# Optimization experiments

Measured on AMD Instinct MI355X. Metric: run time of the kernel, lower is better.

## Reference

```python
import jax, jax.numpy as jnp
import numpy as np

N_USERS = 100000
N_ITEMS = 50000
N_NODES = N_USERS + N_ITEMS
EMB_DIM = 64
NNZ = 4800000
BATCH = 4096
N_LAYERS = 3


def setup_inputs() -> dict:
    key = jax.random.key(0)
    k1, k2, k3, k4, k5, k6, k7, k8 = jax.random.split(key, 8)
    edge_row = jax.random.randint(k1, (NNZ,), 0, N_NODES, dtype=jnp.int32)
    edge_col = jax.random.randint(k2, (NNZ,), 0, N_NODES, dtype=jnp.int32)
    # normalized adjacency values are positive, ~1/sqrt(deg_i*deg_j)
    edge_val = jax.random.uniform(k3, (NNZ,), dtype=jnp.float32) * (2.0 / 32.0)
    user_emb = jax.random.normal(k4, (N_USERS, EMB_DIM), dtype=jnp.float32) * 0.1
    item_emb = jax.random.normal(k5, (N_ITEMS, EMB_DIM), dtype=jnp.float32) * 0.1
    users = jax.random.randint(k6, (BATCH,), 0, N_USERS, dtype=jnp.int64)
    pos_items = jax.random.randint(k7, (BATCH,), 0, N_ITEMS, dtype=jnp.int64)
    neg_items = jax.random.randint(k8, (BATCH,), 0, N_ITEMS, dtype=jnp.int64)
    return {
        "edge_row": edge_row,
        "edge_col": edge_col,
        "edge_val": edge_val,
        "user_emb": user_emb,
        "item_emb": item_emb,
        "users": users,
        "pos_items": pos_items,
        "neg_items": neg_items,
    }


def reference(edge_row, edge_col, edge_val, user_emb, item_emb, users, pos_items, neg_items):
    n_users = user_emb.shape[0]
    n_nodes = n_users + item_emb.shape[0]
    # ego embeddings: [N, D]
    ego = jnp.concatenate([user_emb, item_emb], axis=0)
    acc = ego  # running sum over layers (layer 0 included)
    for _ in range(N_LAYERS):
        # SpMM: out[r] = sum_{e: row[e]==r} val[e] * ego[col[e]]
        msg = edge_val[:, None] * ego[edge_col]          # [nnz, D]
        ego = jax.ops.segment_sum(msg, edge_row, num_segments=n_nodes)
        acc = acc + ego
    all_emb = acc / (N_LAYERS + 1)                       # layer average
    u_all = all_emb[:n_users]
    i_all = all_emb[n_users:]
    u_g = u_all[users]
    pos_i_g = i_all[pos_items]
    neg_i_g = i_all[neg_items]
    return (u_g, pos_i_g, neg_i_g)
```

## Files before the change

kernel.cpp:

```cpp
#include <hip/hip_runtime.h>

#define N_USERS 100000
#define N_ITEMS 50000
#define N_NODES 150000
#define EMB 64
#define NNZ_TOT 4800000
#define BATCH_SZ 4096

#define BROWS 64
#define NB 2344
#define CHUNKS 512
#define CHUNKE 9375
#define SBUF 3072
#define KBINS 2048
#define BIN_LDS (2 * NB * 4 + CHUNKE * 8)
#define QSCALE 262144.0f
#define QINV   3.814697265625e-6f

typedef unsigned short u16;

static __device__ __forceinline__ u16 f2bf(float f) {
    unsigned u = __float_as_uint(f);
    unsigned r = u + 0x7FFFu + ((u >> 16) & 1u);
    return (u16)(r >> 16);
}
static __device__ __forceinline__ float bf2f(u16 h) {
    return __uint_as_float(((unsigned)h) << 16);
}

__global__ void k_init(const float* __restrict__ ue, const float* __restrict__ ie,
                       u16* __restrict__ ego) {
    size_t i = (size_t)blockIdx.x * blockDim.x + threadIdx.x;
    const size_t n4 = (size_t)N_NODES * EMB / 4;
    if (i >= n4) return;
    const size_t u4 = (size_t)N_USERS * EMB / 4;
    float4 v = (i < u4) ? ((const float4*)ue)[i] : ((const float4*)ie)[i - u4];
    ushort4 o;
    o.x = f2bf(v.x); o.y = f2bf(v.y); o.z = f2bf(v.z); o.w = f2bf(v.w);
    ((ushort4*)ego)[i] = o;
}

__global__ void k_zero(int* __restrict__ p, int n) {
    int i = blockIdx.x * blockDim.x + threadIdx.x;
    if (i < n) p[i] = 0;
}

__global__ __launch_bounds__(1024) void k_bin(const int* __restrict__ erow,
                                              const int* __restrict__ ecol,
                                              const float* __restrict__ eval_,
                                              int2* __restrict__ pairsA,
                                              int* __restrict__ off_t,
                                              int* __restrict__ bucketCnt) {
    extern __shared__ int smem[];
    int*  hist = smem;
    int*  fill = smem + NB;
    int2* buf  = (int2*)(smem + 2 * NB);
    const int c = blockIdx.x;
    const int cbase = c * CHUNKE;
    const int tid = threadIdx.x;

    for (int i = tid; i < NB; i += 1024) hist[i] = 0;
    __syncthreads();

    for (int i = tid; i < CHUNKE; i += 1024)
        atomicAdd(&hist[erow[cbase + i] >> 6], 1);
    __syncthreads();

    if (tid < 64) {
        int carry = 0;
        for (int blk = 0; blk < (NB + 63) / 64; ++blk) {
            int idx = blk * 64 + tid;
            int v = (idx < NB) ? hist[idx] : 0;
            int s = v;
            #pragma unroll
            for (int o = 1; o < 64; o <<= 1) {
                int t = __shfl_up(s, o);
                if (tid >= o) s += t;
            }
            if (idx < NB) fill[idx] = s - v + carry;
            carry += __shfl(s, 63);
        }
    }
    __syncthreads();

    for (int i = tid; i < NB; i += 1024) {
        off_t[i * CHUNKS + c] = cbase + fill[i];
        atomicAdd(&bucketCnt[i], hist[i]);
    }
    if (tid == 0) off_t[NB * CHUNKS + c] = cbase + CHUNKE;
    __syncthreads();

    for (int i = tid; i < CHUNKE; i += 1024) {
        int e = cbase + i;
        int r = erow[e];
        int bb = r >> 6;
        int p = atomicAdd(&fill[bb], 1);
        int2 pr;
        pr.x = ((r & 63) << 18) | ecol[e];
        pr.y = __float_as_int(eval_[e]);
        buf[p] = pr;
    }
    __syncthreads();

    for (int i = tid; i < CHUNKE; i += 1024)
        pairsA[cbase + i] = buf[i];
}

__global__ __launch_bounds__(1024) void k_bscan(const int* __restrict__ cnt,
                                                int* __restrict__ bbase,
                                                int* __restrict__ rowptr) {
    __shared__ int lds[1024];
    const int tid = threadIdx.x;
    int vals[3];
    int local = 0;
    #pragma unroll
    for (int j = 0; j < 3; ++j) {
        int idx = tid * 3 + j;
        int v = (idx < NB) ? cnt[idx] : 0;
        vals[j] = local;
        local += v;
    }
    lds[tid] = local;
    __syncthreads();
    for (int off = 1; off < 1024; off <<= 1) {
        int t = (tid >= off) ? lds[tid - off] : 0;
        __syncthreads();
        lds[tid] += t;
        __syncthreads();
    }
    int excl = lds[tid] - local;
    #pragma unroll
    for (int j = 0; j < 3; ++j) {
        int idx = tid * 3 + j;
        if (idx <= NB) {
            int b = excl + vals[j];
            bbase[idx] = b;
            if (idx == NB) rowptr[N_NODES] = b;
        }
    }
}

__global__ __launch_bounds__(256) void k_sort(const int* __restrict__ off_t,
                                              const int2* __restrict__ pairsA,
                                              const int* __restrict__ bbase,
                                              unsigned* __restrict__ pairsB,
                                              int* __restrict__ rowptr) {
    __shared__ int hist[KBINS];
    __shared__ int fillx[KBINS];
    __shared__ int2 buf[SBUF];
    __shared__ int wsum[4];
    const int b = blockIdx.x;
    const int tid = threadIdx.x, lane = tid & 63, w = tid >> 6;

    const int s0 = off_t[b * CHUNKS + tid];
    const int e0 = off_t[(b + 1) * CHUNKS + tid];
    const int s1 = off_t[b * CHUNKS + tid + 256];
    const int e1 = off_t[(b + 1) * CHUNKS + tid + 256];
    const int l0 = e0 - s0;
    const int len = l0 + (e1 - s1);

    for (int i = tid; i < KBINS; i += 256) hist[i] = 0;

    int sc = len;
    #pragma unroll
    for (int o = 1; o < 64; o <<= 1) {
        int t = __shfl_up(sc, o);
        if (lane >= o) sc += t;
    }
    if (lane == 63) wsum[w] = sc;
    __syncthreads();
    int wbase = 0;
    for (int i = 0; i < w; ++i) wbase += wsum[i];
    int tbase = wbase + sc - len;

    for (int i = 0; i < len; ++i) {
        int2 p = (i < l0) ? pairsA[s0 + i] : pairsA[s1 + (i - l0)];
        int dst = tbase + i;
        if (dst < SBUF) buf[dst] = p;
        atomicAdd(&hist[(p.x >> 13) & (KBINS - 1)], 1);
    }
    __syncthreads();

    const int base = bbase[b];
    if (tid < 64) {
        int carry = 0;
        for (int blk = 0; blk < KBINS / 64; ++blk) {
            int idx = blk * 64 + tid;
            int v = hist[idx];
            int s2 = v;
            #pragma unroll
            for (int o = 1; o < 64; o <<= 1) {
                int t = __shfl_up(s2, o);
                if (tid >= o) s2 += t;
            }
            int excl = s2 - v + carry;
            fillx[idx] = excl;
            if ((idx & 31) == 0) {
                int node = b * BROWS + (idx >> 5);
                if (node < N_NODES) rowptr[node] = base + excl;
            }
            carry += __shfl(s2, 63);
        }
    }
    __syncthreads();

    int total = bbase[b + 1] - base;
    if (total > SBUF) total = SBUF;
    for (int i = tid; i < total; i += 256) {
        int2 p = buf[i];
        int pos = atomicAdd(&fillx[(p.x >> 13) & (KBINS - 1)], 1);
        float v = __uint_as_float((unsigned)p.y);
        unsigned q = (unsigned)(v * QSCALE);
        if (q > 16383u) q = 16383u;
        pairsB[base + pos] = (q << 18) | ((unsigned)p.x & 0x3FFFFu);
    }
}

__global__ __launch_bounds__(256) void k_spmv(const int* __restrict__ rowptr,
                                              const unsigned* __restrict__ pairs,
                                              const u16* __restrict__ cur,
                                              u16* __restrict__ nxt) {
    size_t gid = (size_t)blockIdx.x * blockDim.x + threadIdx.x;
    int pr   = (int)(gid >> 6);
    int lane = (int)(gid & 63);
    int rowA = pr * 2;
    if (rowA >= N_NODES) return;
    const int      sl  = lane & 31;
    const bool     hi  = lane >= 32;
    const unsigned sl4 = (unsigned)sl << 2;
    const char* tab = (const char*)cur;
    const uint2* p2 = (const uint2*)pairs;

    int sA = rowptr[rowA];
    int mA = rowptr[rowA + 1];
    int eBnd = rowptr[rowA + 2];

    float a0 = 0.f, a1 = 0.f, b0 = 0.f, b1 = 0.f;
    float c0 = 0.f, c1 = 0.f, d0 = 0.f, d1 = 0.f;

#define PROC1(wv, x0, x1)                                                      \
    {                                                                          \
        unsigned col = (wv) & 0x3FFFFu;                                        \
        float v = (float)((wv) >> 18) * QINV;                                  \
        unsigned u = *(const unsigned*)(tab + (size_t)((col << 7) | sl4));     \
        float vm = hi ? 0.f : v;                                               \
        x0 += vm * __uint_as_float(u << 16);                                   \
        x1 += vm * __uint_as_float(u & 0xFFFF0000u);                           \
    }
#define PROC(d, x0, x1)                                                        \
    {                                                                          \
        unsigned wv = hi ? (d).y : (d).x;                                      \
        unsigned col = wv & 0x3FFFFu;                                          \
        float vv = (float)(wv >> 18) * QINV;                                   \
        unsigned u = *(const unsigned*)(tab + (size_t)((col << 7) | sl4));     \
        x0 += vv * __uint_as_float(u << 16);                                   \
        x1 += vv * __uint_as_float(u & 0xFFFF0000u);                           \
    }

    int eA = sA, eB = mA;
    if ((eA & 1) && eA < mA)   { unsigned q = pairs[eA]; PROC1(q, a0, a1) ++eA; }
    if ((eB & 1) && eB < eBnd) { unsigned q = pairs[eB]; PROC1(q, c0, c1) ++eB; }

    while (eA + 7 < mA && eB + 7 < eBnd) {
        int hA = eA >> 1, hB = eB >> 1;
        uint2 A0 = p2[hA + 0], A1 = p2[hA + 1], A2 = p2[hA + 2], A3 = p2[hA + 3];
        uint2 B0 = p2[hB + 0], B1 = p2[hB + 1], B2 = p2[hB + 2], B3 = p2[hB + 3];
        PROC(A0, a0, a1) PROC(B0, c0, c1)
        PROC(A1, b0, b1) PROC(B1, d0, d1)
        PROC(A2, a0, a1) PROC(B2, c0, c1)
        PROC(A3, b0, b1) PROC(B3, d0, d1)
        eA += 8; eB += 8;
    }
    for (; eA + 7 < mA; eA += 8) {
        int h = eA >> 1;
        uint2 q0 = p2[h + 0], q1 = p2[h + 1], q2 = p2[h + 2], q3 = p2[h + 3];
        PROC(q0, a0, a1) PROC(q1, b0, b1) PROC(q2, a0, a1) PROC(q3, b0, b1)
    }
    for (; eA + 1 < mA; eA += 2) {
        uint2 d = p2[eA >> 1];
        PROC(d, a0, a1)
    }
    if (eA < mA) { unsigned q = pairs[eA]; PROC1(q, a0, a1) }
    for (; eB + 7 < eBnd; eB += 8) {
        int h = eB >> 1;
        uint2 q0 = p2[h + 0], q1 = p2[h + 1], q2 = p2[h + 2], q3 = p2[h + 3];
        PROC(q0, c0, c1) PROC(q1, d0, d1) PROC(q2, c0, c1) PROC(q3, d0, d1)
    }
    for (; eB + 1 < eBnd; eB += 2) {
        uint2 d = p2[eB >> 1];
        PROC(d, c0, c1)
    }
    if (eB < eBnd) { unsigned q = pairs[eB]; PROC1(q, c0, c1) }
#undef PROC
#undef PROC1

    float s0 = a0 + b0, s1 = a1 + b1;
    float t0 = c0 + d0, t1 = c1 + d1;
    s0 += __shfl_xor(s0, 32);
    s1 += __shfl_xor(s1, 32);
    t0 += __shfl_xor(t0, 32);
    t1 += __shfl_xor(t1, 32);
    if (!hi) {
        unsigned oA = (unsigned)f2bf(s0) | ((unsigned)f2bf(s1) << 16);
        unsigned oB = (unsigned)f2bf(t0) | ((unsigned)f2bf(t1) << 16);
        ((unsigned*)nxt)[(size_t)rowA * 32 + sl] = oA;
        ((unsigned*)nxt)[(size_t)(rowA + 1) * 32 + sl] = oB;
    }
}

__global__ void k_out0(const float* __restrict__ ue, const float* __restrict__ ie,
                       const int* __restrict__ users, const int* __restrict__ pos,
                       const int* __restrict__ neg, float* __restrict__ out) {
    size_t t = (size_t)blockIdx.x * blockDim.x + threadIdx.x;
    size_t r = t >> 4;
    int sub = (int)(t & 15);
    if (r >= (size_t)(3 * BATCH_SZ)) return;
    int which = (int)(r / BATCH_SZ);
    int bi    = (int)(r % BATCH_SZ);
    int node;
    if (which == 0)      node = users[bi];
    else if (which == 1) node = N_USERS + pos[bi];
    else                 node = N_USERS + neg[bi];
    const float* src = (node < N_USERS) ? (ue + (size_t)node * EMB)
                                        : (ie + (size_t)(node - N_USERS) * EMB);
    float4 v = ((const float4*)src)[sub];
    ((float4*)(out + r * EMB))[sub] = v;
}

__global__ void k_outb(const u16* __restrict__ ego,
                       const int* __restrict__ users, const int* __restrict__ pos,
                       const int* __restrict__ neg, float* __restrict__ out) {
    size_t t = (size_t)blockIdx.x * blockDim.x + threadIdx.x;
    size_t r = t >> 4;
    int sub = (int)(t & 15);
    if (r >= (size_t)(3 * BATCH_SZ)) return;
    int which = (int)(r / BATCH_SZ);
    int bi    = (int)(r % BATCH_SZ);
    int node;
    if (which == 0)      node = users[bi];
    else if (which == 1) node = N_USERS + pos[bi];
    else                 node = N_USERS + neg[bi];
    ushort4 h = ((const ushort4*)(ego + (size_t)node * EMB))[sub];
    float4* op = (float4*)(out + r * EMB) + sub;
    float4 o = *op;
    o.x += bf2f(h.x); o.y += bf2f(h.y); o.z += bf2f(h.z); o.w += bf2f(h.w);
    *op = o;
}

#define RFL(x) __builtin_amdgcn_readfirstlane(x)
__global__ __launch_bounds__(256) void k_last(const int* __restrict__ rowptr,
                                              const unsigned* __restrict__ pairs,
                                              const u16* __restrict__ cur,
                                              const int* __restrict__ users,
                                              const int* __restrict__ pos,
                                              const int* __restrict__ neg,
                                              float* __restrict__ out) {
    size_t gid = (size_t)blockIdx.x * blockDim.x + threadIdx.x;
    int r    = (int)(gid >> 6);
    int lane = (int)(gid & 63);
    if (r >= 3 * BATCH_SZ) return;
    int which = r / BATCH_SZ;
    int bi    = r % BATCH_SZ;
    int node;
    if (which == 0)      node = users[bi];
    else if (which == 1) node = N_USERS + pos[bi];
    else                 node = N_USERS + neg[bi];
    int start = rowptr[node];
    int end   = rowptr[node + 1];
    float a0 = 0.f, a1 = 0.f, a2 = 0.f, a3 = 0.f;
    int e = start;
    for (; e + 3 < end; e += 4) {
        unsigned w0 = RFL(pairs[e]);
        unsigned w1 = RFL(pairs[e + 1]);
        unsigned w2 = RFL(pairs[e + 2]);
        unsigned w3 = RFL(pairs[e + 3]);
        float v0 = (float)(w0 >> 18) * QINV;
        float v1 = (float)(w1 >> 18) * QINV;
        float v2 = (float)(w2 >> 18) * QINV;
        float v3 = (float)(w3 >> 18) * QINV;
        a0 += v0 * bf2f(cur[(size_t)(w0 & 0x3FFFFu) * EMB + lane]);
        a1 += v1 * bf2f(cur[(size_t)(w1 & 0x3FFFFu) * EMB + lane]);
        a2 += v2 * bf2f(cur[(size_t)(w2 & 0x3FFFFu) * EMB + lane]);
        a3 += v3 * bf2f(cur[(size_t)(w3 & 0x3FFFFu) * EMB + lane]);
    }
    for (; e < end; ++e) {
        unsigned w = RFL(pairs[e]);
        float v = (float)(w >> 18) * QINV;
        a0 += v * bf2f(cur[(size_t)(w & 0x3FFFFu) * EMB + lane]);
    }
    float sum = (a0 + a1) + (a2 + a3);
    size_t oi = (size_t)r * EMB + lane;
    out[oi] = (out[oi] + sum) * 0.25f;
}

extern "C" void kernel_launch(void* const* d_in, const int* in_sizes, int n_in,
                              void* d_out, int out_size, void* d_ws, size_t ws_size,
                              hipStream_t stream) {
    const int*   erow  = (const int*)  d_in[0];
    const int*   ecol  = (const int*)  d_in[1];
    const float* eval_ = (const float*)d_in[2];
    const float* ue    = (const float*)d_in[3];
    const float* ie    = (const float*)d_in[4];
    const int*   users = (const int*)  d_in[5];
    const int*   pos   = (const int*)  d_in[6];
    const int*   neg   = (const int*)  d_in[7];
    float* out = (float*)d_out;

    char* ws = (char*)d_ws;
    const size_t tblB  = (size_t)150016 * EMB * sizeof(u16);
    const size_t pairB = (size_t)NNZ_TOT * sizeof(int2);
    u16*  ego0   = (u16*)(ws);
    u16*  ego1   = (u16*)(ws + tblB);
    int2* pairsA = (int2*)(ws);
    unsigned* pairsB = (unsigned*)(ws + 2 * tblB);
    int*  off_t  = (int*) (ws + 2 * tblB + pairB);
    int*  rowptr = off_t + (size_t)(NB + 1) * CHUNKS;
    int*  bucketCnt = rowptr + ((N_NODES + 1 + 63) & ~63);
    int*  bbase     = bucketCnt + NB;

    const int blk = 256;

    hipFuncSetAttribute(reinterpret_cast<const void*>(k_bin),
                        hipFuncAttributeMaxDynamicSharedMemorySize, BIN_LDS);

    k_zero<<<(NB + blk - 1) / blk, blk, 0, stream>>>(bucketCnt, NB);
    k_bin<<<CHUNKS, 1024, BIN_LDS, stream>>>(erow, ecol, eval_, pairsA, off_t, bucketCnt);
    k_bscan<<<1, 1024, 0, stream>>>(bucketCnt, bbase, rowptr);
    k_sort<<<NB, blk, 0, stream>>>(off_t, pairsA, bbase, pairsB, rowptr);

    const size_t n4 = (size_t)N_NODES * EMB / 4;
    k_init<<<(int)((n4 + blk - 1) / blk), blk, 0, stream>>>(ue, ie, ego0);

    const int grid_g = (int)(((size_t)3 * BATCH_SZ * 16 + blk - 1) / blk);
    k_out0<<<grid_g, blk, 0, stream>>>(ue, ie, users, pos, neg, out);

    const size_t spmv_threads = (size_t)(N_NODES / 2) * 64;
    const int grid_spmv = (int)((spmv_threads + blk - 1) / blk);
    k_spmv<<<grid_spmv, blk, 0, stream>>>(rowptr, pairsB, ego0, ego1);
    k_outb<<<grid_g, blk, 0, stream>>>(ego1, users, pos, neg, out);
    k_spmv<<<grid_spmv, blk, 0, stream>>>(rowptr, pairsB, ego1, ego0);
    k_outb<<<grid_g, blk, 0, stream>>>(ego0, users, pos, neg, out);

    const size_t lth = (size_t)3 * BATCH_SZ * 64;
    k_last<<<(int)((lth + blk - 1) / blk), blk, 0, stream>>>(rowptr, pairsB, ego0,
                                                             users, pos, neg, out);
}
```

Baseline: 388.1 us.

## Load-balance edge gathering in sort kernel and bucket by row only

Previously each thread serially walked its own two input segments into the block's buffer. Now all threads cooperatively scan the block's output range, binary-searching a shared table of segment offsets to find each element's source index. This balances the uneven segment lengths across threads and makes the global loads closer to coalesced. The counting sort also drops from 2048 bins (row plus a coarse column sub-bucket) to 64 bins (row only), which shortens the scan. The cost is that edges within a row are no longer grouped by column, which may reduce cache locality of the embedding gathers in the SpMV passes.

After: 334.1 us. 1.16x faster.

```diff
diff --git a/kernel.cpp b/kernel.cpp
--- a/kernel.cpp
+++ b/kernel.cpp
@@ -12,7 +12,6 @@
 #define CHUNKS 512
 #define CHUNKE 9375
 #define SBUF 3072
-#define KBINS 2048
 #define BIN_LDS (2 * NB * 4 + CHUNKE * 8)
 #define QSCALE 262144.0f
 #define QINV   3.814697265625e-6f
@@ -145,8 +144,10 @@
                                               const int* __restrict__ bbase,
                                               unsigned* __restrict__ pairsB,
                                               int* __restrict__ rowptr) {
-    __shared__ int hist[KBINS];
-    __shared__ int fillx[KBINS];
+    __shared__ int hist[BROWS];
+    __shared__ int fillx[BROWS];
+    __shared__ int segstart[2 * CHUNKS / 2];
+    __shared__ int segbase[2 * CHUNKS / 2];
     __shared__ int2 buf[SBUF];
     __shared__ int wsum[4];
     const int b = blockIdx.x;
@@ -159,7 +160,7 @@
     const int l0 = e0 - s0;
     const int len = l0 + (e1 - s1);
 
-    for (int i = tid; i < KBINS; i += 256) hist[i] = 0;
+    if (tid < BROWS) hist[tid] = 0;
 
     int sc = len;
     #pragma unroll
@@ -173,42 +174,70 @@
     for (int i = 0; i < w; ++i) wbase += wsum[i];
     int tbase = wbase + sc - len;
 
-    for (int i = 0; i < len; ++i) {
-        int2 p = (i < l0) ? pairsA[s0 + i] : pairsA[s1 + (i - l0)];
-        int dst = tbase + i;
-        if (dst < SBUF) buf[dst] = p;
-        atomicAdd(&hist[(p.x >> 13) & (KBINS - 1)], 1);
-    }
+    segbase[2 * tid]     = tbase;
+    segbase[2 * tid + 1] = tbase + l0;
+    segstart[2 * tid]     = s0;
+    segstart[2 * tid + 1] = s1;
     __syncthreads();
 
     const int base = bbase[b];
-    if (tid < 64) {
-        int carry = 0;
-        for (int blk = 0; blk < KBINS / 64; ++blk) {
-            int idx = blk * 64 + tid;
-            int v = hist[idx];
-            int s2 = v;
-            #pragma unroll
-            for (int o = 1; o < 64; o <<= 1) {
-                int t = __shfl_up(s2, o);
-                if (tid >= o) s2 += t;
-            }
-            int excl = s2 - v + carry;
-            fillx[idx] = excl;
-            if ((idx & 31) == 0) {
-                int node = b * BROWS + (idx >> 5);
-                if (node < N_NODES) rowptr[node] = base + excl;
-            }
-            carry += __shfl(s2, 63);
-        }
-    }
-    __syncthreads();
-
     int total = bbase[b + 1] - base;
     if (total > SBUF) total = SBUF;
+
+#define FINDSEG(j, idx)                                                        \
+    {                                                                          \
+        int lo = 0, hi = 511;                                                  \
+        while (lo < hi) {                                                      \
+            int mid = (lo + hi + 1) >> 1;                                      \
+            if (segbase[mid] <= (j)) lo = mid; else hi = mid - 1;              \
+        }                                                                      \
+        (idx) = segstart[lo] + ((j) - segbase[lo]);                            \
+    }
+
+    int j = tid;
+    for (; j + 768 < total; j += 1024) {
+        int i0, i1, i2, i3;
+        FINDSEG(j,       i0)
+        FINDSEG(j + 256, i1)
+        FINDSEG(j + 512, i2)
+        FINDSEG(j + 768, i3)
+        int2 p0 = pairsA[i0];
+        int2 p1 = pairsA[i1];
+        int2 p2 = pairsA[i2];
+        int2 p3 = pairsA[i3];
+        buf[j]       = p0; atomicAdd(&hist[p0.x >> 18], 1);
+        buf[j + 256] = p1; atomicAdd(&hist[p1.x >> 18], 1);
+        buf[j + 512] = p2; atomicAdd(&hist[p2.x >> 18], 1);
+        buf[j + 768] = p3; atomicAdd(&hist[p3.x >> 18], 1);
+    }
+    for (; j < total; j += 256) {
+        int idx;
+        FINDSEG(j, idx)
+        int2 p = pairsA[idx];
+        buf[j] = p;
+        atomicAdd(&hist[p.x >> 18], 1);
+    }
+#undef FINDSEG
+    __syncthreads();
+
+    if (tid < 64) {
+        int v = hist[tid];
+        int s2 = v;
+        #pragma unroll
+        for (int o = 1; o < 64; o <<= 1) {
+            int t = __shfl_up(s2, o);
+            if (tid >= o) s2 += t;
+        }
+        int excl = s2 - v;
+        fillx[tid] = excl;
+        int node = b * BROWS + tid;
+        if (node < N_NODES) rowptr[node] = base + excl;
+    }
+    __syncthreads();
+
     for (int i = tid; i < total; i += 256) {
         int2 p = buf[i];
-        int pos = atomicAdd(&fillx[(p.x >> 13) & (KBINS - 1)], 1);
+        int pos = atomicAdd(&fillx[p.x >> 18], 1);
         float v = __uint_as_float((unsigned)p.y);
         unsigned q = (unsigned)(v * QSCALE);
         if (q > 16383u) q = 16383u;
```
